# Kernel optimization log

Measured on AMD Instinct MI355X. Metric: run time of the kernel, lower is better.

Reference implementation:

```python
import jax, jax.numpy as jnp
import numpy as np

DIM = 128
HEADS = 4
K = 7          # neighborhood kernel size
MLP_RATIO = 4
EPS = 1e-5


def setup_inputs() -> dict:
    key = jax.random.key(0)
    ks = jax.random.split(key, 8)
    B, H, W, C = 4, 64, 64, DIM
    hid = C * MLP_RATIO
    s = lambda k, shape: jax.random.normal(k, shape, jnp.float32) * 0.02
    return {
        "x": jax.random.normal(ks[0], (B, H, W, C), jnp.float32),
        "ln1_g": jnp.ones((C,), jnp.float32),
        "ln1_b": jnp.zeros((C,), jnp.float32),
        "qkv_w": s(ks[1], (C, 3 * C)),
        "qkv_b": jnp.zeros((3 * C,), jnp.float32),
        "rpb": s(ks[2], (HEADS, 2 * K - 1, 2 * K - 1)),
        "proj_w": s(ks[3], (C, C)),
        "proj_b": jnp.zeros((C,), jnp.float32),
        "ln2_g": jnp.ones((C,), jnp.float32),
        "ln2_b": jnp.zeros((C,), jnp.float32),
        "fc1_w": s(ks[4], (C, hid)),
        "fc1_b": jnp.zeros((hid,), jnp.float32),
        "fc2_w": s(ks[5], (hid, C)),
        "fc2_b": jnp.zeros((C,), jnp.float32),
    }


def _ln(x, g, b):
    m = jnp.mean(x, axis=-1, keepdims=True)
    v = jnp.mean(jnp.square(x - m), axis=-1, keepdims=True)
    return (x - m) * jax.lax.rsqrt(v + EPS) * g + b


def _neigh_idx(L, k):
    # NATTEN border-clamped neighborhood: start = clamp(i - k//2, 0, L-k)
    i = jnp.arange(L)
    start = jnp.clip(i - k // 2, 0, L - k)
    idx = start[:, None] + jnp.arange(k)[None, :]        # [L, k] key positions
    rel = idx - i[:, None] + (k - 1)                     # [L, k] rpb indices in [0, 2k-2]
    return idx, rel


def _neighborhood_attention(x, qkv_w, qkv_b, rpb, proj_w, proj_b):
    B, H, W, C = x.shape
    nh, hd = HEADS, C // HEADS
    scale = hd ** -0.5
    qkv = (x @ qkv_w + qkv_b).reshape(B, H, W, 3, nh, hd)
    qkv = qkv.transpose(3, 0, 4, 1, 2, 5)                # [3, B, nh, H, W, hd]
    q, k_, v = qkv[0] * scale, qkv[1], qkv[2]
    ih, rh = _neigh_idx(H, K)
    iw, rw = _neigh_idx(W, K)
    # gather 7x7 neighborhoods: [B, nh, H, K, W, K, hd]
    kg = k_[:, :, ih][:, :, :, :, iw]
    vg = v[:, :, ih][:, :, :, :, iw]
    attn = jnp.einsum('bnywc,bnykxjc->bnyxkj', q, kg)    # [B, nh, H, W, K, K]
    bias = rpb[:, rh][:, :, :, rw]                       # [nh, H, K, W, K]
    attn = attn + bias.transpose(0, 1, 3, 2, 4)[None]
    a = jax.nn.softmax(attn.reshape(B, nh, H, W, K * K), axis=-1)
    a = a.reshape(B, nh, H, W, K, K)
    out = jnp.einsum('bnyxkj,bnykxjc->bnyxc', a, vg)     # [B, nh, H, W, hd]
    out = out.transpose(0, 2, 3, 1, 4).reshape(B, H, W, C)
    return out @ proj_w + proj_b


def reference(x, ln1_g, ln1_b, qkv_w, qkv_b, rpb, proj_w, proj_b,
              ln2_g, ln2_b, fc1_w, fc1_b, fc2_w, fc2_b):
    h = x + _neighborhood_attention(_ln(x, ln1_g, ln1_b), qkv_w, qkv_b, rpb, proj_w, proj_b)
    y = _ln(h, ln2_g, ln2_b)
    y = jax.nn.gelu(y @ fc1_w + fc1_b, approximate=False) @ fc2_w + fc2_b
    return h + y
```

## Files before the change

### kernel.cpp

```cpp
#include <hip/hip_runtime.h>
#include <math.h>

#define TOKS 16384
#define CDIM 128
#define NH 4
#define HD 32
#define HID 512
#define QSCALE 0.17677669529663687f
#define LEPS 1e-5f

typedef const float* fp;
typedef const unsigned short* bfp16;
typedef __attribute__((ext_vector_type(8))) short bf16x8;
typedef __attribute__((ext_vector_type(4))) float f32x4;

__device__ inline unsigned int bfp2(float a, float b) {
    unsigned int ua = __float_as_uint(a); ua = (ua + 0x7FFFu + ((ua >> 16) & 1u)) >> 16;
    unsigned int ub = __float_as_uint(b); ub = (ub + 0x7FFFu + ((ub >> 16) & 1u)) >> 16;
    return ua | (ub << 16);
}
__device__ inline unsigned short bf1(float a) {
    unsigned int u = __float_as_uint(a);
    return (unsigned short)((u + 0x7FFFu + ((u >> 16) & 1u)) >> 16);
}
__device__ inline float lo16(unsigned int u) { return __uint_as_float(u << 16); }
__device__ inline float hi16(unsigned int u) { return __uint_as_float(u & 0xFFFF0000u); }

__global__ __launch_bounds__(256) void prep(fp qw, fp pw, fp f1w, fp f2w,
                                            unsigned short* __restrict__ wt) {
    int e = blockIdx.x * 256 + threadIdx.x;
    float v;
    if (e < 49152)       { int n = e >> 7,  k = e & 127;          v = qw[(size_t)k * 384 + n]; }
    else if (e < 65536)  { int i = e - 49152;  int n = i >> 7, k = i & 127; v = pw[(size_t)k * 128 + n]; }
    else if (e < 131072) { int i = e - 65536;  int n = i >> 7, k = i & 127; v = f1w[(size_t)k * 512 + n]; }
    else                 { int i = e - 131072; int n = i >> 9, k = i & 511; v = f2w[(size_t)k * 128 + n]; }
    wt[e] = bf1(v);
}

__global__ __launch_bounds__(256) void k1_mfma(fp x, fp g1, fp b1, bfp16 wt0, fp wb,
                                               float* __restrict__ qb,
                                               unsigned short* __restrict__ kvb) {
    __shared__ unsigned int lds[12288];
    const int m0 = blockIdx.x * 128;
    const int nb = blockIdx.y * 64;
    const int tid = threadIdx.x;
#pragma unroll
    for (int i = 0; i < 8; i++) {
        int slot = tid + i * 256;
        int m = slot >> 4, c16 = slot & 15;
        const float4 v0 = *(const float4*)(x + (size_t)(m0 + m) * CDIM + c16 * 8);
        const float4 v1 = *(const float4*)(x + (size_t)(m0 + m) * CDIM + c16 * 8 + 4);
        float s = v0.x + v0.y + v0.z + v0.w + v1.x + v1.y + v1.z + v1.w;
        float q = v0.x * v0.x + v0.y * v0.y + v0.z * v0.z + v0.w * v0.w
                + v1.x * v1.x + v1.y * v1.y + v1.z * v1.z + v1.w * v1.w;
#pragma unroll
        for (int mm = 8; mm >= 1; mm >>= 1) { s += __shfl_xor(s, mm); q += __shfl_xor(q, mm); }
        float mu = s * (1.f / 128.f);
        float rs = rsqrtf(q * (1.f / 128.f) - mu * mu + LEPS);
        const float4 ga = *(const float4*)(g1 + c16 * 8);
        const float4 gb = *(const float4*)(g1 + c16 * 8 + 4);
        const float4 ba = *(const float4*)(b1 + c16 * 8);
        const float4 bb = *(const float4*)(b1 + c16 * 8 + 4);
        uint4 o;
        o.x = bfp2((v0.x - mu) * rs * ga.x + ba.x, (v0.y - mu) * rs * ga.y + ba.y);
        o.y = bfp2((v0.z - mu) * rs * ga.z + ba.z, (v0.w - mu) * rs * ga.w + ba.w);
        o.z = bfp2((v1.x - mu) * rs * gb.x + bb.x, (v1.y - mu) * rs * gb.y + bb.y);
        o.w = bfp2((v1.z - mu) * rs * gb.z + bb.z, (v1.w - mu) * rs * gb.w + bb.w);
        *(uint4*)&lds[m * 64 + ((c16 ^ (m & 15)) << 2)] = o;
    }
#pragma unroll
    for (int i = 0; i < 4; i++) {
        int slot = tid + i * 256;
        int n = slot >> 4, c16 = slot & 15;
        const uint4 v4 = *(const uint4*)(wt0 + (size_t)(nb + n) * 128 + c16 * 8);
        *(uint4*)&lds[8192 + n * 64 + (c16 ^ (n & 15)) * 4] = v4;
    }
    __syncthreads();

    const int lane = tid & 63, wid = tid >> 6, quad = lane >> 4, l16 = lane & 15;
    f32x4 acc[2][4];
#pragma unroll
    for (int mt = 0; mt < 2; mt++)
#pragma unroll
        for (int nt = 0; nt < 4; nt++) acc[mt][nt] = (f32x4){0.f, 0.f, 0.f, 0.f};
#pragma unroll
    for (int kk = 0; kk < 4; kk++) {
        int c = kk * 4 + quad;
        bf16x8 a0 = *(bf16x8*)&lds[(wid * 32 + l16) * 64 + (c ^ l16) * 4];
        bf16x8 a1 = *(bf16x8*)&lds[(wid * 32 + 16 + l16) * 64 + (c ^ l16) * 4];
#pragma unroll
        for (int nt = 0; nt < 4; nt++) {
            bf16x8 bf = *(bf16x8*)&lds[8192 + (nt * 16 + l16) * 64 + (c ^ l16) * 4];
            acc[0][nt] = __builtin_amdgcn_mfma_f32_16x16x32_bf16(a0, bf, acc[0][nt], 0, 0, 0);
            acc[1][nt] = __builtin_amdgcn_mfma_f32_16x16x32_bf16(a1, bf, acc[1][nt], 0, 0, 0);
        }
    }
#pragma unroll
    for (int nt = 0; nt < 4; nt++) {
        int col = nb + nt * 16 + l16;
        float bias = wb[col];
#pragma unroll
        for (int mt = 0; mt < 2; mt++)
#pragma unroll
            for (int r = 0; r < 4; r++) {
                int row = m0 + wid * 32 + mt * 16 + quad * 4 + r;
                float vres = acc[mt][nt][r] + bias;
                if (col < 128)
                    qb[(size_t)row * 128 + col] = vres * QSCALE;
                else if (col < 256)
                    kvb[(size_t)row * 256 + (col - 128)] = bf1(vres);
                else
                    kvb[(size_t)row * 256 + 128 + (col - 256)] = bf1(vres);
            }
    }
}

__global__ __launch_bounds__(512) void k2_attn(const float* __restrict__ qb,
                                               const unsigned short* __restrict__ kvb,
                                               fp rpb, unsigned short* __restrict__ attnb) {
    __shared__ unsigned int lds[25088];
    const int tile = blockIdx.x;
    const int bb = tile >> 6;
    const int ty0 = ((tile >> 3) & 7) << 3;
    const int tx0 = (tile & 7) << 3;
    const int ry0 = min(max(ty0 - 3, 0), 50);
    const int rx0 = min(max(tx0 - 3, 0), 50);
    const int tid = threadIdx.x;

#pragma unroll
    for (int it = 0; it < 13; it++) {
        int slot = it * 512 + tid;
        if (slot < 6272) {
            int r = slot >> 5, c = slot & 31;
            int i = r / 14, j = r - i * 14;
            const uint4 v = *(const uint4*)(kvb + (size_t)((bb << 12) + (ry0 + i) * 64 + rx0 + j) * 256 + c * 8);
            *(uint4*)&lds[r * 128 + ((c ^ (r & 7)) << 2)] = v;
        }
    }

    const int dh = tid & 1;
    const int head = (tid >> 1) & 3;
    const int t = tid >> 3;
    const int tx = t & 7, ty = t >> 3;
    const int y = ty0 + ty, x = tx0 + tx;
    const int token = (bb << 12) + y * 64 + x;
    const int sy = min(max(y - 3, 0), 57);
    const int sx = min(max(x - 3, 0), 57);
    const int ib = sy - ry0, jb = sx - rx0;
    const float* rp = rpb + head * 169 + (sy - y + 6) * 13 + (sx - x + 6);

    float q[16];
    {
        const float4* qp = (const float4*)(qb + (size_t)token * 128 + head * 32 + dh * 16);
        float4 a = qp[0], b = qp[1], c = qp[2], d = qp[3];
        q[0] = a.x; q[1] = a.y; q[2] = a.z; q[3] = a.w;
        q[4] = b.x; q[5] = b.y; q[6] = b.z; q[7] = b.w;
        q[8] = c.x; q[9] = c.y; q[10] = c.z; q[11] = c.w;
        q[12] = d.x; q[13] = d.y; q[14] = d.z; q[15] = d.w;
    }
    __syncthreads();

    const int cb = (head << 2) + (dh << 1);
    float m = -1e30f, l = 0.f;
    float o[16];
#pragma unroll
    for (int i2 = 0; i2 < 16; i2++) o[i2] = 0.f;

    for (int dy = 0; dy < 7; dy++) {
        float s[7];
#pragma unroll
        for (int dx = 0; dx < 7; dx++) {
            int r = (ib + dy) * 14 + jb + dx;
            int sw = r & 7;
            const uint4 k0 = *(const uint4*)&lds[r * 128 + ((cb ^ sw) << 2)];
            const uint4 k1 = *(const uint4*)&lds[r * 128 + (((cb + 1) ^ sw) << 2)];
            float ss = q[0] * lo16(k0.x) + q[1] * hi16(k0.x)
                     + q[2] * lo16(k0.y) + q[3] * hi16(k0.y)
                     + q[4] * lo16(k0.z) + q[5] * hi16(k0.z)
                     + q[6] * lo16(k0.w) + q[7] * hi16(k0.w)
                     + q[8] * lo16(k1.x) + q[9] * hi16(k1.x)
                     + q[10] * lo16(k1.y) + q[11] * hi16(k1.y)
                     + q[12] * lo16(k1.z) + q[13] * hi16(k1.z)
                     + q[14] * lo16(k1.w) + q[15] * hi16(k1.w);
            ss += __shfl_xor(ss, 1);
            s[dx] = ss + rp[dy * 13 + dx];
        }
        float rm = s[0];
#pragma unroll
        for (int dx = 1; dx < 7; dx++) rm = fmaxf(rm, s[dx]);
        float mn = fmaxf(m, rm);
        float cf = __expf(m - mn);
        l *= cf;
#pragma unroll
        for (int i2 = 0; i2 < 16; i2++) o[i2] *= cf;
#pragma unroll
        for (int dx = 0; dx < 7; dx++) {
            int r = (ib + dy) * 14 + jb + dx;
            int sw = r & 7;
            const uint4 v0 = *(const uint4*)&lds[r * 128 + (((cb + 16) ^ sw) << 2)];
            const uint4 v1 = *(const uint4*)&lds[r * 128 + (((cb + 17) ^ sw) << 2)];
            float p = __expf(s[dx] - mn);
            l += p;
            o[0] += p * lo16(v0.x); o[1] += p * hi16(v0.x);
            o[2] += p * lo16(v0.y); o[3] += p * hi16(v0.y);
            o[4] += p * lo16(v0.z); o[5] += p * hi16(v0.z);
            o[6] += p * lo16(v0.w); o[7] += p * hi16(v0.w);
            o[8] += p * lo16(v1.x); o[9] += p * hi16(v1.x);
            o[10] += p * lo16(v1.y); o[11] += p * hi16(v1.y);
            o[12] += p * lo16(v1.z); o[13] += p * hi16(v1.z);
            o[14] += p * lo16(v1.w); o[15] += p * hi16(v1.w);
        }
        m = mn;
    }
    float inv = 1.f / l;
    unsigned short* op = attnb + (size_t)token * 128 + head * 32 + dh * 16;
    uint4 ov;
    ov.x = bfp2(o[0] * inv, o[1] * inv); ov.y = bfp2(o[2] * inv, o[3] * inv);
    ov.z = bfp2(o[4] * inv, o[5] * inv); ov.w = bfp2(o[6] * inv, o[7] * inv);
    *(uint4*)op = ov;
    ov.x = bfp2(o[8] * inv, o[9] * inv); ov.y = bfp2(o[10] * inv, o[11] * inv);
    ov.z = bfp2(o[12] * inv, o[13] * inv); ov.w = bfp2(o[14] * inv, o[15] * inv);
    *(uint4*)(op + 8) = ov;
}

__global__ __launch_bounds__(256) void k3_mfma(bfp16 attnb, fp x, bfp16 wt1, fp pb,
                                               fp g2, fp b2,
                                               float* __restrict__ h,
                                               unsigned short* __restrict__ hn) {
    __shared__ unsigned int lds[12288];
    const int m0 = blockIdx.x * 64;
    const int tid = threadIdx.x;
#pragma unroll
    for (int i = 0; i < 4; i++) {
        int slot = tid + i * 256;
        int m = slot >> 4, c16 = slot & 15;
        const uint4 v4 = *(const uint4*)(attnb + (size_t)(m0 + m) * CDIM + c16 * 8);
        *(uint4*)&lds[m * 64 + (c16 ^ (m & 15)) * 4] = v4;
    }
#pragma unroll
    for (int i = 0; i < 8; i++) {
        int slot = tid + i * 256;
        int n = slot >> 4, c16 = slot & 15;
        const uint4 v4 = *(const uint4*)(wt1 + (size_t)n * 128 + c16 * 8);
        *(uint4*)&lds[4096 + n * 64 + (c16 ^ (n & 15)) * 4] = v4;
    }
    __syncthreads();

    const int lane = tid & 63, wid = tid >> 6, quad = lane >> 4, l16 = lane & 15;
    const int mrow = wid * 16 + l16;
    f32x4 acc[8];
#pragma unroll
    for (int nt = 0; nt < 8; nt++) acc[nt] = (f32x4){0.f, 0.f, 0.f, 0.f};
#pragma unroll
    for (int kk = 0; kk < 4; kk++) {
        int c = kk * 4 + quad;
        bf16x8 a = *(bf16x8*)&lds[mrow * 64 + (c ^ l16) * 4];
#pragma unroll
        for (int nt = 0; nt < 8; nt++) {
            bf16x8 bf = *(bf16x8*)&lds[4096 + (nt * 16 + l16) * 64 + (c ^ l16) * 4];
            acc[nt] = __builtin_amdgcn_mfma_f32_16x16x32_bf16(a, bf, acc[nt], 0, 0, 0);
        }
    }
    float s[4] = {0.f, 0.f, 0.f, 0.f}, q[4] = {0.f, 0.f, 0.f, 0.f};
#pragma unroll
    for (int nt = 0; nt < 8; nt++) {
        int col = nt * 16 + l16;
        float bias = pb[col];
#pragma unroll
        for (int r = 0; r < 4; r++) {
            int row = m0 + wid * 16 + quad * 4 + r;
            float hv = x[(size_t)row * CDIM + col] + acc[nt][r] + bias;
            h[(size_t)row * CDIM + col] = hv;
            acc[nt][r] = hv;
            s[r] += hv; q[r] += hv * hv;
        }
    }
#pragma unroll
    for (int m = 1; m <= 8; m <<= 1) {
#pragma unroll
        for (int r = 0; r < 4; r++) {
            s[r] += __shfl_xor(s[r], m);
            q[r] += __shfl_xor(q[r], m);
        }
    }
    float mu[4], rs[4];
#pragma unroll
    for (int r = 0; r < 4; r++) {
        mu[r] = s[r] * (1.f / 128.f);
        rs[r] = rsqrtf(q[r] * (1.f / 128.f) - mu[r] * mu[r] + LEPS);
    }
#pragma unroll
    for (int nt = 0; nt < 8; nt++) {
        int col = nt * 16 + l16;
        float gg = g2[col], bb = b2[col];
#pragma unroll
        for (int r = 0; r < 4; r++) {
            int row = m0 + wid * 16 + quad * 4 + r;
            hn[(size_t)row * CDIM + col] = bf1((acc[nt][r] - mu[r]) * rs[r] * gg + bb);
        }
    }
}

__global__ __launch_bounds__(256) void kmlp3(bfp16 hn, bfp16 wt2, fp b1v, bfp16 wt3, fp b2v,
                                             fp h, float* __restrict__ out) {
    __shared__ unsigned int lds[10240];
    const int m0 = blockIdx.x * 32;
    const int tid = threadIdx.x;
#pragma unroll
    for (int i = 0; i < 2; i++) {
        int slot = tid + i * 256;
        int m = slot >> 4, c16 = slot & 15;
        const uint4 v4 = *(const uint4*)(hn + (size_t)(m0 + m) * CDIM + c16 * 8);
        *(uint4*)&lds[m * 64 + ((c16 ^ (m & 15)) << 2)] = v4;
    }
    __syncthreads();

    const int lane = tid & 63, wid = tid >> 6, quad = lane >> 4, l16 = lane & 15;

#pragma unroll
    for (int ht = 0; ht < 8; ht++) {
        const int hrow = wid * 128 + ht * 16 + l16;
        f32x4 acc0 = (f32x4){0.f, 0.f, 0.f, 0.f};
        f32x4 acc1 = (f32x4){0.f, 0.f, 0.f, 0.f};
#pragma unroll
        for (int kk = 0; kk < 4; kk++) {
            int c = kk * 4 + quad;
            bf16x8 wf = *(const bf16x8*)(wt2 + (size_t)hrow * 128 + kk * 32 + quad * 8);
            bf16x8 x0 = *(bf16x8*)&lds[l16 * 64 + ((c ^ l16) << 2)];
            bf16x8 x1 = *(bf16x8*)&lds[(16 + l16) * 64 + ((c ^ l16) << 2)];
            acc0 = __builtin_amdgcn_mfma_f32_16x16x32_bf16(wf, x0, acc0, 0, 0, 0);
            acc1 = __builtin_amdgcn_mfma_f32_16x16x32_bf16(wf, x1, acc1, 0, 0, 0);
        }
        const int hidb = wid * 128 + ht * 16 + quad * 4;
        const float4 bb = *(const float4*)(b1v + hidb);
        const int c16y = hidb >> 3;
        const int woff = (quad & 1) << 1;
#pragma unroll
        for (int t = 0; t < 2; t++) {
            f32x4 a = t ? acc1 : acc0;
            int row = t * 16 + l16;
            float z0 = a[0] + bb.x, z1 = a[1] + bb.y, z2 = a[2] + bb.z, z3 = a[3] + bb.w;
            float g0 = 0.5f * z0 * (1.f + erff(z0 * 0.70710678118654752f));
            float g1 = 0.5f * z1 * (1.f + erff(z1 * 0.70710678118654752f));
            float g2 = 0.5f * z2 * (1.f + erff(z2 * 0.70710678118654752f));
            float g3 = 0.5f * z3 * (1.f + erff(z3 * 0.70710678118654752f));
            uint2 val; val.x = bfp2(g0, g1); val.y = bfp2(g2, g3);
            *(uint2*)&lds[2048 + row * 256 + ((c16y ^ (row & 15)) << 2) + woff] = val;
        }
    }
    __syncthreads();

    f32x4 acc2[2][2];
#pragma unroll
    for (int mt = 0; mt < 2; mt++)
#pragma unroll
        for (int nt = 0; nt < 2; nt++) acc2[mt][nt] = (f32x4){0.f, 0.f, 0.f, 0.f};
#pragma unroll
    for (int kc = 0; kc < 16; kc++) {
        int c = kc * 4 + quad;
        bf16x8 a0 = *(bf16x8*)&lds[2048 + l16 * 256 + ((c ^ l16) << 2)];
        bf16x8 a1 = *(bf16x8*)&lds[2048 + (16 + l16) * 256 + ((c ^ l16) << 2)];
#pragma unroll
        for (int nt = 0; nt < 2; nt++) {
            int crow = wid * 32 + nt * 16 + l16;
            bf16x8 bf = *(const bf16x8*)(wt3 + (size_t)crow * 512 + kc * 32 + quad * 8);
            acc2[0][nt] = __builtin_amdgcn_mfma_f32_16x16x32_bf16(a0, bf, acc2[0][nt], 0, 0, 0);
            acc2[1][nt] = __builtin_amdgcn_mfma_f32_16x16x32_bf16(a1, bf, acc2[1][nt], 0, 0, 0);
        }
    }
#pragma unroll
    for (int nt = 0; nt < 2; nt++) {
        int col = wid * 32 + nt * 16 + l16;
        float bias = b2v[col];
#pragma unroll
        for (int mt = 0; mt < 2; mt++)
#pragma unroll
            for (int r = 0; r < 4; r++) {
                int row = m0 + mt * 16 + quad * 4 + r;
                out[(size_t)row * CDIM + col] = h[(size_t)row * CDIM + col] + acc2[mt][nt][r] + bias;
            }
    }
}

extern "C" void kernel_launch(void* const* d_in, const int* in_sizes, int n_in,
                              void* d_out, int out_size, void* d_ws, size_t ws_size,
                              hipStream_t stream) {
    fp x      = (fp)d_in[0];
    fp ln1_g  = (fp)d_in[1];
    fp ln1_b  = (fp)d_in[2];
    fp qkv_w  = (fp)d_in[3];
    fp qkv_b  = (fp)d_in[4];
    fp rpb    = (fp)d_in[5];
    fp proj_w = (fp)d_in[6];
    fp proj_b = (fp)d_in[7];
    fp ln2_g  = (fp)d_in[8];
    fp ln2_b  = (fp)d_in[9];
    fp fc1_w  = (fp)d_in[10];
    fp fc1_b  = (fp)d_in[11];
    fp fc2_w  = (fp)d_in[12];
    fp fc2_b  = (fp)d_in[13];
    float* out = (float*)d_out;

    float* ws = (float*)d_ws;
    float* h  = ws;
    unsigned short* xn = (unsigned short*)(h + (size_t)TOKS * CDIM);
    unsigned short* hn = xn + (size_t)TOKS * CDIM;
    float* qb = (float*)(hn + (size_t)TOKS * CDIM);
    unsigned short* kvb   = (unsigned short*)(qb + (size_t)TOKS * CDIM);
    unsigned short* attnb = kvb + (size_t)TOKS * 256;
    unsigned short* wt    = attnb + (size_t)TOKS * CDIM;

    unsigned short* wt0 = wt;
    unsigned short* wt1 = wt + 49152;
    unsigned short* wt2 = wt + 65536;
    unsigned short* wt3 = wt + 131072;

    prep<<<768, 256, 0, stream>>>(qkv_w, proj_w, fc1_w, fc2_w, wt);
    k1_mfma<<<dim3(TOKS / 128, 6), 256, 0, stream>>>(x, ln1_g, ln1_b, wt0, qkv_b, qb, kvb);
    k2_attn<<<TOKS / 64, 512, 0, stream>>>(qb, kvb, rpb, attnb);
    k3_mfma<<<TOKS / 64, 256, 0, stream>>>(attnb, x, wt1, proj_b, ln2_g, ln2_b, h, hn);
    kmlp3<<<TOKS / 32, 256, 0, stream>>>(hn, wt2, fc1_b, wt3, fc2_b, h, out);
}
```

Measured before the change: 143.9 us.

## Fuse output projection, residual and LayerNorm2 into the neighborhood attention kernel

The attention kernel now stages its per-tile 64x128 bf16 output in LDS together with the projection weights, which are prefetched into registers at kernel start. Half the threads then run the MFMA projection, add the residual, compute LayerNorm2 and write h and hn directly. This drops the separate k3 launch and the global round trip of the attention output. In exchange it adds register pressure in the attention kernel, and the epilogue runs on only 256 of 512 threads, which may reduce occupancy or overlap.

```diff
diff --git a/kernel.cpp b/kernel.cpp
--- a/kernel.cpp
+++ b/kernel.cpp
@@ -117,7 +117,10 @@
 
 __global__ __launch_bounds__(512) void k2_attn(const float* __restrict__ qb,
                                                const unsigned short* __restrict__ kvb,
-                                               fp rpb, unsigned short* __restrict__ attnb) {
+                                               fp rpb, fp x, bfp16 wt1, fp pb,
+                                               fp g2, fp b2,
+                                               float* __restrict__ h,
+                                               unsigned short* __restrict__ hn) {
     __shared__ unsigned int lds[25088];
     const int tile = blockIdx.x;
     const int bb = tile >> 6;
@@ -126,6 +129,12 @@
     const int ry0 = min(max(ty0 - 3, 0), 50);
     const int rx0 = min(max(tx0 - 3, 0), 50);
     const int tid = threadIdx.x;
+    const int base = (bb << 12) + ty0 * 64 + tx0;
+
+    uint4 wreg[4];
+#pragma unroll
+    for (int i = 0; i < 4; i++)
+        wreg[i] = *(const uint4*)(wt1 + (size_t)(tid + i * 512) * 8);
 
 #pragma unroll
     for (int it = 0; it < 13; it++) {
@@ -142,12 +151,12 @@
     const int head = (tid >> 1) & 3;
     const int t = tid >> 3;
     const int tx = t & 7, ty = t >> 3;
-    const int y = ty0 + ty, x = tx0 + tx;
-    const int token = (bb << 12) + y * 64 + x;
+    const int y = ty0 + ty, xx2 = tx0 + tx;
+    const int token = (bb << 12) + y * 64 + xx2;
     const int sy = min(max(y - 3, 0), 57);
-    const int sx = min(max(x - 3, 0), 57);
+    const int sx = min(max(xx2 - 3, 0), 57);
     const int ib = sy - ry0, jb = sx - rx0;
-    const float* rp = rpb + head * 169 + (sy - y + 6) * 13 + (sx - x + 6);
+    const float* rp = rpb + head * 169 + (sy - y + 6) * 13 + (sx - xx2 + 6);
 
     float q[16];
     {
@@ -213,90 +222,79 @@
         m = mn;
     }
     float inv = 1.f / l;
-    unsigned short* op = attnb + (size_t)token * 128 + head * 32 + dh * 16;
-    uint4 ov;
-    ov.x = bfp2(o[0] * inv, o[1] * inv); ov.y = bfp2(o[2] * inv, o[3] * inv);
-    ov.z = bfp2(o[4] * inv, o[5] * inv); ov.w = bfp2(o[6] * inv, o[7] * inv);
-    *(uint4*)op = ov;
-    ov.x = bfp2(o[8] * inv, o[9] * inv); ov.y = bfp2(o[10] * inv, o[11] * inv);
-    ov.z = bfp2(o[12] * inv, o[13] * inv); ov.w = bfp2(o[14] * inv, o[15] * inv);
-    *(uint4*)(op + 8) = ov;
-}
-
-__global__ __launch_bounds__(256) void k3_mfma(bfp16 attnb, fp x, bfp16 wt1, fp pb,
-                                               fp g2, fp b2,
-                                               float* __restrict__ h,
-                                               unsigned short* __restrict__ hn) {
-    __shared__ unsigned int lds[12288];
-    const int m0 = blockIdx.x * 64;
-    const int tid = threadIdx.x;
+    uint4 ov0, ov1;
+    ov0.x = bfp2(o[0] * inv, o[1] * inv);  ov0.y = bfp2(o[2] * inv, o[3] * inv);
+    ov0.z = bfp2(o[4] * inv, o[5] * inv);  ov0.w = bfp2(o[6] * inv, o[7] * inv);
+    ov1.x = bfp2(o[8] * inv, o[9] * inv);  ov1.y = bfp2(o[10] * inv, o[11] * inv);
+    ov1.z = bfp2(o[12] * inv, o[13] * inv); ov1.w = bfp2(o[14] * inv, o[15] * inv);
+
+    __syncthreads();
+    *(uint4*)&lds[t * 64 + ((cb ^ (t & 15)) << 2)] = ov0;
+    *(uint4*)&lds[t * 64 + (((cb + 1) ^ (t & 15)) << 2)] = ov1;
 #pragma unroll
     for (int i = 0; i < 4; i++) {
-        int slot = tid + i * 256;
-        int m = slot >> 4, c16 = slot & 15;
-        const uint4 v4 = *(const uint4*)(attnb + (size_t)(m0 + m) * CDIM + c16 * 8);
-        *(uint4*)&lds[m * 64 + (c16 ^ (m & 15)) * 4] = v4;
-    }
-#pragma unroll
-    for (int i = 0; i < 8; i++) {
-        int slot = tid + i * 256;
+        int slot = tid + i * 512;
         int n = slot >> 4, c16 = slot & 15;
-        const uint4 v4 = *(const uint4*)(wt1 + (size_t)n * 128 + c16 * 8);
-        *(uint4*)&lds[4096 + n * 64 + (c16 ^ (n & 15)) * 4] = v4;
-    }
-    __syncthreads();
-
-    const int lane = tid & 63, wid = tid >> 6, quad = lane >> 4, l16 = lane & 15;
-    const int mrow = wid * 16 + l16;
-    f32x4 acc[8];
-#pragma unroll
-    for (int nt = 0; nt < 8; nt++) acc[nt] = (f32x4){0.f, 0.f, 0.f, 0.f};
-#pragma unroll
-    for (int kk = 0; kk < 4; kk++) {
-        int c = kk * 4 + quad;
-        bf16x8 a = *(bf16x8*)&lds[mrow * 64 + (c ^ l16) * 4];
+        *(uint4*)&lds[4096 + n * 64 + ((c16 ^ (n & 15)) << 2)] = wreg[i];
+    }
+    __syncthreads();
+
+    if (tid < 256) {
+        const int lane2 = tid & 63, wid2 = tid >> 6, quad2 = lane2 >> 4, l162 = lane2 & 15;
+        const int mrow = wid2 * 16 + l162;
+        f32x4 acc[8];
+#pragma unroll
+        for (int nt = 0; nt < 8; nt++) acc[nt] = (f32x4){0.f, 0.f, 0.f, 0.f};
+#pragma unroll
+        for (int kk = 0; kk < 4; kk++) {
+            int c = kk * 4 + quad2;
+            bf16x8 a = *(bf16x8*)&lds[mrow * 64 + ((c ^ l162) << 2)];
+#pragma unroll
+            for (int nt = 0; nt < 8; nt++) {
+                bf16x8 bf = *(bf16x8*)&lds[4096 + (nt * 16 + l162) * 64 + ((c ^ l162) << 2)];
+                acc[nt] = __builtin_amdgcn_mfma_f32_16x16x32_bf16(a, bf, acc[nt], 0, 0, 0);
+            }
+        }
+        float s2[4] = {0.f, 0.f, 0.f, 0.f}, q2[4] = {0.f, 0.f, 0.f, 0.f};
+        int grow[4];
+#pragma unroll
+        for (int r = 0; r < 4; r++) {
+            int lt = wid2 * 16 + quad2 * 4 + r;
+            grow[r] = base + ((lt >> 3) << 6) + (lt & 7);
+        }
 #pragma unroll
         for (int nt = 0; nt < 8; nt++) {
-            bf16x8 bf = *(bf16x8*)&lds[4096 + (nt * 16 + l16) * 64 + (c ^ l16) * 4];
-            acc[nt] = __builtin_amdgcn_mfma_f32_16x16x32_bf16(a, bf, acc[nt], 0, 0, 0);
-        }
-    }
-    float s[4] = {0.f, 0.f, 0.f, 0.f}, q[4] = {0.f, 0.f, 0.f, 0.f};
-#pragma unroll
-    for (int nt = 0; nt < 8; nt++) {
-        int col = nt * 16 + l16;
-        float bias = pb[col];
+            int col = nt * 16 + l162;
+            float bias = pb[col];
+#pragma unroll
+            for (int r = 0; r < 4; r++) {
+                float hv = x[(size_t)grow[r] * CDIM + col] + acc[nt][r] + bias;
+                h[(size_t)grow[r] * CDIM + col] = hv;
+                acc[nt][r] = hv;
+                s2[r] += hv; q2[r] += hv * hv;
+            }
+        }
+#pragma unroll
+        for (int mm = 1; mm <= 8; mm <<= 1) {
+#pragma unroll
+            for (int r = 0; r < 4; r++) {
+                s2[r] += __shfl_xor(s2[r], mm);
+                q2[r] += __shfl_xor(q2[r], mm);
+            }
+        }
+        float mu[4], rs[4];
 #pragma unroll
         for (int r = 0; r < 4; r++) {
-            int row = m0 + wid * 16 + quad * 4 + r;
-            float hv = x[(size_t)row * CDIM + col] + acc[nt][r] + bias;
-            h[(size_t)row * CDIM + col] = hv;
-            acc[nt][r] = hv;
-            s[r] += hv; q[r] += hv * hv;
-        }
-    }
-#pragma unroll
-    for (int m = 1; m <= 8; m <<= 1) {
-#pragma unroll
-        for (int r = 0; r < 4; r++) {
-            s[r] += __shfl_xor(s[r], m);
-            q[r] += __shfl_xor(q[r], m);
-        }
-    }
-    float mu[4], rs[4];
-#pragma unroll
-    for (int r = 0; r < 4; r++) {
-        mu[r] = s[r] * (1.f / 128.f);
-        rs[r] = rsqrtf(q[r] * (1.f / 128.f) - mu[r] * mu[r] + LEPS);
-    }
-#pragma unroll
-    for (int nt = 0; nt < 8; nt++) {
-        int col = nt * 16 + l16;
-        float gg = g2[col], bb = b2[col];
-#pragma unroll
-        for (int r = 0; r < 4; r++) {
-            int row = m0 + wid * 16 + quad * 4 + r;
-            hn[(size_t)row * CDIM + col] = bf1((acc[nt][r] - mu[r]) * rs[r] * gg + bb);
+            mu[r] = s2[r] * (1.f / 128.f);
+            rs[r] = rsqrtf(q2[r] * (1.f / 128.f) - mu[r] * mu[r] + LEPS);
+        }
+#pragma unroll
+        for (int nt = 0; nt < 8; nt++) {
+            int col = nt * 16 + l162;
+            float gg = g2[col], bbv = b2[col];
+#pragma unroll
+            for (int r = 0; r < 4; r++)
+                hn[(size_t)grow[r] * CDIM + col] = bf1((acc[nt][r] - mu[r]) * rs[r] * gg + bbv);
         }
     }
 }
@@ -417,7 +415,6 @@
 
     prep<<<768, 256, 0, stream>>>(qkv_w, proj_w, fc1_w, fc2_w, wt);
     k1_mfma<<<dim3(TOKS / 128, 6), 256, 0, stream>>>(x, ln1_g, ln1_b, wt0, qkv_b, qb, kvb);
-    k2_attn<<<TOKS / 64, 512, 0, stream>>>(qb, kvb, rpb, attnb);
-    k3_mfma<<<TOKS / 64, 256, 0, stream>>>(attnb, x, wt1, proj_b, ln2_g, ln2_b, h, hn);
+    k2_attn<<<TOKS / 64, 512, 0, stream>>>(qb, kvb, rpb, x, wt1, proj_b, ln2_g, ln2_b, h, hn);
     kmlp3<<<TOKS / 32, 256, 0, stream>>>(hn, wt2, fc1_b, wt3, fc2_b, h, out);
 }
```

Result: slower. 164.1 us (+14.0%).

## Split neighborhood attention blocks per head with smaller LDS tiles

Applied to the files above, without the earlier changes.

The attention kernel now launches one block per (tile, head) pair instead of one block covering all four heads. Each block stages only that head's K/V slice (8 KB per row tile instead of 32 KB) into shared memory and uses 256 threads, with each head-dim quarter handled by one thread and a two-step shuffle reduction. This aims to raise occupancy and block count (smaller LDS, fewer registers) at the cost of an extra shuffle and more, smaller global loads of the halo region.

```diff
diff --git a/kernel.cpp b/kernel.cpp
--- a/kernel.cpp
+++ b/kernel.cpp
@@ -115,11 +115,13 @@
     }
 }
 
-__global__ __launch_bounds__(512) void k2_attn(const float* __restrict__ qb,
+__global__ __launch_bounds__(256) void k2_attn(const float* __restrict__ qb,
                                                const unsigned short* __restrict__ kvb,
                                                fp rpb, unsigned short* __restrict__ attnb) {
-    __shared__ unsigned int lds[25088];
-    const int tile = blockIdx.x;
+    __shared__ unsigned int lds[6272];
+    const int blk = blockIdx.x;
+    const int head = blk & 3;
+    const int tile = blk >> 2;
     const int bb = tile >> 6;
     const int ty0 = ((tile >> 3) & 7) << 3;
     const int tx0 = (tile & 7) << 3;
@@ -128,19 +130,20 @@
     const int tid = threadIdx.x;
 
 #pragma unroll
-    for (int it = 0; it < 13; it++) {
-        int slot = it * 512 + tid;
-        if (slot < 6272) {
-            int r = slot >> 5, c = slot & 31;
+    for (int it = 0; it < 7; it++) {
+        int slot = it * 256 + tid;
+        if (slot < 1568) {
+            int r = slot >> 3, c = slot & 7;
             int i = r / 14, j = r - i * 14;
-            const uint4 v = *(const uint4*)(kvb + (size_t)((bb << 12) + (ry0 + i) * 64 + rx0 + j) * 256 + c * 8);
-            *(uint4*)&lds[r * 128 + ((c ^ (r & 7)) << 2)] = v;
-        }
-    }
-
-    const int dh = tid & 1;
-    const int head = (tid >> 1) & 3;
-    const int t = tid >> 3;
+            size_t tok = (size_t)((bb << 12) + (ry0 + i) * 64 + rx0 + j);
+            int off = (c < 4) ? (head * 32 + c * 8) : (128 + head * 32 + (c - 4) * 8);
+            const uint4 v = *(const uint4*)(kvb + tok * 256 + off);
+            *(uint4*)&lds[r * 32 + ((c ^ (r & 7)) << 2)] = v;
+        }
+    }
+
+    const int dh = tid & 3;
+    const int t = tid >> 2;
     const int tx = t & 7, ty = t >> 3;
     const int y = ty0 + ty, x = tx0 + tx;
     const int token = (bb << 12) + y * 64 + x;
@@ -149,40 +152,32 @@
     const int ib = sy - ry0, jb = sx - rx0;
     const float* rp = rpb + head * 169 + (sy - y + 6) * 13 + (sx - x + 6);
 
-    float q[16];
+    float q[8];
     {
-        const float4* qp = (const float4*)(qb + (size_t)token * 128 + head * 32 + dh * 16);
-        float4 a = qp[0], b = qp[1], c = qp[2], d = qp[3];
-        q[0] = a.x; q[1] = a.y; q[2] = a.z; q[3] = a.w;
-        q[4] = b.x; q[5] = b.y; q[6] = b.z; q[7] = b.w;
-        q[8] = c.x; q[9] = c.y; q[10] = c.z; q[11] = c.w;
-        q[12] = d.x; q[13] = d.y; q[14] = d.z; q[15] = d.w;
+        const float4* qp = (const float4*)(qb + (size_t)token * 128 + head * 32 + dh * 8);
+        float4 q0 = qp[0], q1 = qp[1];
+        q[0] = q0.x; q[1] = q0.y; q[2] = q0.z; q[3] = q0.w;
+        q[4] = q1.x; q[5] = q1.y; q[6] = q1.z; q[7] = q1.w;
     }
     __syncthreads();
 
-    const int cb = (head << 2) + (dh << 1);
     float m = -1e30f, l = 0.f;
-    float o[16];
-#pragma unroll
-    for (int i2 = 0; i2 < 16; i2++) o[i2] = 0.f;
+    float o[8];
+#pragma unroll
+    for (int i2 = 0; i2 < 8; i2++) o[i2] = 0.f;
 
     for (int dy = 0; dy < 7; dy++) {
         float s[7];
 #pragma unroll
         for (int dx = 0; dx < 7; dx++) {
             int r = (ib + dy) * 14 + jb + dx;
-            int sw = r & 7;
-            const uint4 k0 = *(const uint4*)&lds[r * 128 + ((cb ^ sw) << 2)];
-            const uint4 k1 = *(const uint4*)&lds[r * 128 + (((cb + 1) ^ sw) << 2)];
-            float ss = q[0] * lo16(k0.x) + q[1] * hi16(k0.x)
-                     + q[2] * lo16(k0.y) + q[3] * hi16(k0.y)
-                     + q[4] * lo16(k0.z) + q[5] * hi16(k0.z)
-                     + q[6] * lo16(k0.w) + q[7] * hi16(k0.w)
-                     + q[8] * lo16(k1.x) + q[9] * hi16(k1.x)
-                     + q[10] * lo16(k1.y) + q[11] * hi16(k1.y)
-                     + q[12] * lo16(k1.z) + q[13] * hi16(k1.z)
-                     + q[14] * lo16(k1.w) + q[15] * hi16(k1.w);
+            const uint4 kk = *(const uint4*)&lds[r * 32 + ((dh ^ (r & 7)) << 2)];
+            float ss = q[0] * lo16(kk.x) + q[1] * hi16(kk.x)
+                     + q[2] * lo16(kk.y) + q[3] * hi16(kk.y)
+                     + q[4] * lo16(kk.z) + q[5] * hi16(kk.z)
+                     + q[6] * lo16(kk.w) + q[7] * hi16(kk.w);
             ss += __shfl_xor(ss, 1);
+            ss += __shfl_xor(ss, 2);
             s[dx] = ss + rp[dy * 13 + dx];
         }
         float rm = s[0];
@@ -192,35 +187,25 @@
         float cf = __expf(m - mn);
         l *= cf;
 #pragma unroll
-        for (int i2 = 0; i2 < 16; i2++) o[i2] *= cf;
+        for (int i2 = 0; i2 < 8; i2++) o[i2] *= cf;
 #pragma unroll
         for (int dx = 0; dx < 7; dx++) {
             int r = (ib + dy) * 14 + jb + dx;
-            int sw = r & 7;
-            const uint4 v0 = *(const uint4*)&lds[r * 128 + (((cb + 16) ^ sw) << 2)];
-            const uint4 v1 = *(const uint4*)&lds[r * 128 + (((cb + 17) ^ sw) << 2)];
+            const uint4 vv = *(const uint4*)&lds[r * 32 + (((4 + dh) ^ (r & 7)) << 2)];
             float p = __expf(s[dx] - mn);
             l += p;
-            o[0] += p * lo16(v0.x); o[1] += p * hi16(v0.x);
-            o[2] += p * lo16(v0.y); o[3] += p * hi16(v0.y);
-            o[4] += p * lo16(v0.z); o[5] += p * hi16(v0.z);
-            o[6] += p * lo16(v0.w); o[7] += p * hi16(v0.w);
-            o[8] += p * lo16(v1.x); o[9] += p * hi16(v1.x);
-            o[10] += p * lo16(v1.y); o[11] += p * hi16(v1.y);
-            o[12] += p * lo16(v1.z); o[13] += p * hi16(v1.z);
-            o[14] += p * lo16(v1.w); o[15] += p * hi16(v1.w);
+            o[0] += p * lo16(vv.x); o[1] += p * hi16(vv.x);
+            o[2] += p * lo16(vv.y); o[3] += p * hi16(vv.y);
+            o[4] += p * lo16(vv.z); o[5] += p * hi16(vv.z);
+            o[6] += p * lo16(vv.w); o[7] += p * hi16(vv.w);
         }
         m = mn;
     }
     float inv = 1.f / l;
-    unsigned short* op = attnb + (size_t)token * 128 + head * 32 + dh * 16;
     uint4 ov;
     ov.x = bfp2(o[0] * inv, o[1] * inv); ov.y = bfp2(o[2] * inv, o[3] * inv);
     ov.z = bfp2(o[4] * inv, o[5] * inv); ov.w = bfp2(o[6] * inv, o[7] * inv);
-    *(uint4*)op = ov;
-    ov.x = bfp2(o[8] * inv, o[9] * inv); ov.y = bfp2(o[10] * inv, o[11] * inv);
-    ov.z = bfp2(o[12] * inv, o[13] * inv); ov.w = bfp2(o[14] * inv, o[15] * inv);
-    *(uint4*)(op + 8) = ov;
+    *(uint4*)(attnb + (size_t)token * 128 + head * 32 + dh * 8) = ov;
 }
 
 __global__ __launch_bounds__(256) void k3_mfma(bfp16 attnb, fp x, bfp16 wt1, fp pb,
@@ -417,7 +402,7 @@
 
     prep<<<768, 256, 0, stream>>>(qkv_w, proj_w, fc1_w, fc2_w, wt);
     k1_mfma<<<dim3(TOKS / 128, 6), 256, 0, stream>>>(x, ln1_g, ln1_b, wt0, qkv_b, qb, kvb);
-    k2_attn<<<TOKS / 64, 512, 0, stream>>>(qb, kvb, rpb, attnb);
+    k2_attn<<<TOKS / 64 * NH, 256, 0, stream>>>(qb, kvb, rpb, attnb);
     k3_mfma<<<TOKS / 64, 256, 0, stream>>>(attnb, x, wt1, proj_b, ln2_g, ln2_b, h, hn);
     kmlp3<<<TOKS / 32, 256, 0, stream>>>(hn, wt2, fc1_b, wt3, fc2_b, h, out);
 }
```

Measured after the change: 147.4 us. 2.5% more time.

## Fuse projection+LN2 kernel with MLP kernel, keeping residual and normed tile in LDS

Applied to the files above, without the earlier changes.

Merges the attention output projection, residual add and LayerNorm2 into the MLP kernel, so each 32-token block computes h and its normalized bf16 copy in shared memory rather than writing them to global memory and reading them back. LN row statistics are now split across two waves per row half and combined through LDS. This removes one kernel launch and the global round trip for h (fp32) and hn (bf16). In exchange, proj weights are read straight from global memory instead of being staged in LDS, and the larger LDS footprint may reduce occupancy.

```diff
diff --git a/kernel.cpp b/kernel.cpp
--- a/kernel.cpp
+++ b/kernel.cpp
@@ -223,99 +223,93 @@
     *(uint4*)(op + 8) = ov;
 }
 
-__global__ __launch_bounds__(256) void k3_mfma(bfp16 attnb, fp x, bfp16 wt1, fp pb,
-                                               fp g2, fp b2,
-                                               float* __restrict__ h,
-                                               unsigned short* __restrict__ hn) {
-    __shared__ unsigned int lds[12288];
-    const int m0 = blockIdx.x * 64;
+__global__ __launch_bounds__(256) void kpm(bfp16 attnb, fp x, bfp16 wt1, fp pb,
+                                           fp g2, fp b2, bfp16 wt2, fp b1v,
+                                           bfp16 wt3, fp b2v, float* __restrict__ out) {
+    __shared__ unsigned int lds[16384];
+    float* ldsf = (float*)lds;
+    unsigned short* ldsu = (unsigned short*)lds;
+    const int m0 = blockIdx.x * 32;
     const int tid = threadIdx.x;
-#pragma unroll
-    for (int i = 0; i < 4; i++) {
+    const int lane = tid & 63, wid = tid >> 6, quad = lane >> 4, l16 = lane & 15;
+
+#pragma unroll
+    for (int i = 0; i < 2; i++) {
         int slot = tid + i * 256;
         int m = slot >> 4, c16 = slot & 15;
         const uint4 v4 = *(const uint4*)(attnb + (size_t)(m0 + m) * CDIM + c16 * 8);
-        *(uint4*)&lds[m * 64 + (c16 ^ (m & 15)) * 4] = v4;
-    }
-#pragma unroll
-    for (int i = 0; i < 8; i++) {
-        int slot = tid + i * 256;
-        int n = slot >> 4, c16 = slot & 15;
-        const uint4 v4 = *(const uint4*)(wt1 + (size_t)n * 128 + c16 * 8);
-        *(uint4*)&lds[4096 + n * 64 + (c16 ^ (n & 15)) * 4] = v4;
-    }
-    __syncthreads();
-
-    const int lane = tid & 63, wid = tid >> 6, quad = lane >> 4, l16 = lane & 15;
-    const int mrow = wid * 16 + l16;
-    f32x4 acc[8];
-#pragma unroll
-    for (int nt = 0; nt < 8; nt++) acc[nt] = (f32x4){0.f, 0.f, 0.f, 0.f};
+        *(uint4*)&lds[m * 64 + ((c16 ^ (m & 15)) << 2)] = v4;
+    }
+    __syncthreads();
+
+    const int mt = wid & 1, nhf = wid >> 1;
+    f32x4 pacc[4];
+#pragma unroll
+    for (int nt = 0; nt < 4; nt++) pacc[nt] = (f32x4){0.f, 0.f, 0.f, 0.f};
 #pragma unroll
     for (int kk = 0; kk < 4; kk++) {
         int c = kk * 4 + quad;
-        bf16x8 a = *(bf16x8*)&lds[mrow * 64 + (c ^ l16) * 4];
-#pragma unroll
-        for (int nt = 0; nt < 8; nt++) {
-            bf16x8 bf = *(bf16x8*)&lds[4096 + (nt * 16 + l16) * 64 + (c ^ l16) * 4];
-            acc[nt] = __builtin_amdgcn_mfma_f32_16x16x32_bf16(a, bf, acc[nt], 0, 0, 0);
-        }
-    }
-    float s[4] = {0.f, 0.f, 0.f, 0.f}, q[4] = {0.f, 0.f, 0.f, 0.f};
-#pragma unroll
-    for (int nt = 0; nt < 8; nt++) {
-        int col = nt * 16 + l16;
+        bf16x8 a = *(bf16x8*)&lds[(mt * 16 + l16) * 64 + ((c ^ l16) << 2)];
+#pragma unroll
+        for (int nt = 0; nt < 4; nt++) {
+            int crow = nhf * 64 + nt * 16 + l16;
+            bf16x8 bf = *(const bf16x8*)(wt1 + (size_t)crow * 128 + kk * 32 + quad * 8);
+            pacc[nt] = __builtin_amdgcn_mfma_f32_16x16x32_bf16(a, bf, pacc[nt], 0, 0, 0);
+        }
+    }
+    float sr[4] = {0.f, 0.f, 0.f, 0.f}, qr[4] = {0.f, 0.f, 0.f, 0.f};
+#pragma unroll
+    for (int nt = 0; nt < 4; nt++) {
+        int col = nhf * 64 + nt * 16 + l16;
         float bias = pb[col];
 #pragma unroll
         for (int r = 0; r < 4; r++) {
-            int row = m0 + wid * 16 + quad * 4 + r;
-            float hv = x[(size_t)row * CDIM + col] + acc[nt][r] + bias;
-            h[(size_t)row * CDIM + col] = hv;
-            acc[nt][r] = hv;
-            s[r] += hv; q[r] += hv * hv;
-        }
-    }
-#pragma unroll
-    for (int m = 1; m <= 8; m <<= 1) {
+            int lrow = mt * 16 + quad * 4 + r;
+            float hv = x[(size_t)(m0 + lrow) * CDIM + col] + pacc[nt][r] + bias;
+            ldsf[4096 + lrow * 128 + col] = hv;
+            pacc[nt][r] = hv;
+            sr[r] += hv; qr[r] += hv * hv;
+        }
+    }
+#pragma unroll
+    for (int mm = 1; mm <= 8; mm <<= 1) {
 #pragma unroll
         for (int r = 0; r < 4; r++) {
-            s[r] += __shfl_xor(s[r], m);
-            q[r] += __shfl_xor(q[r], m);
-        }
-    }
+            sr[r] += __shfl_xor(sr[r], mm);
+            qr[r] += __shfl_xor(qr[r], mm);
+        }
+    }
+    __syncthreads();
+    if (l16 == 0) {
+#pragma unroll
+        for (int r = 0; r < 4; r++) {
+            ldsf[wid * 32 + (quad * 4 + r) * 2]     = sr[r];
+            ldsf[wid * 32 + (quad * 4 + r) * 2 + 1] = qr[r];
+        }
+    }
+    __syncthreads();
     float mu[4], rs[4];
 #pragma unroll
     for (int r = 0; r < 4; r++) {
-        mu[r] = s[r] * (1.f / 128.f);
-        rs[r] = rsqrtf(q[r] * (1.f / 128.f) - mu[r] * mu[r] + LEPS);
-    }
-#pragma unroll
-    for (int nt = 0; nt < 8; nt++) {
-        int col = nt * 16 + l16;
-        float gg = g2[col], bb = b2[col];
+        int po = (wid ^ 2) * 32 + (quad * 4 + r) * 2;
+        float st = sr[r] + ldsf[po];
+        float qt = qr[r] + ldsf[po + 1];
+        mu[r] = st * (1.f / 128.f);
+        rs[r] = rsqrtf(qt * (1.f / 128.f) - mu[r] * mu[r] + LEPS);
+    }
+#pragma unroll
+    for (int nt = 0; nt < 4; nt++) {
+        int col = nhf * 64 + nt * 16 + l16;
+        float gg = g2[col], bbv = b2[col];
+        int c16h = col >> 3, cw = col & 7;
 #pragma unroll
         for (int r = 0; r < 4; r++) {
-            int row = m0 + wid * 16 + quad * 4 + r;
-            hn[(size_t)row * CDIM + col] = bf1((acc[nt][r] - mu[r]) * rs[r] * gg + bb);
-        }
-    }
-}
-
-__global__ __launch_bounds__(256) void kmlp3(bfp16 hn, bfp16 wt2, fp b1v, bfp16 wt3, fp b2v,
-                                             fp h, float* __restrict__ out) {
-    __shared__ unsigned int lds[10240];
-    const int m0 = blockIdx.x * 32;
-    const int tid = threadIdx.x;
-#pragma unroll
-    for (int i = 0; i < 2; i++) {
-        int slot = tid + i * 256;
-        int m = slot >> 4, c16 = slot & 15;
-        const uint4 v4 = *(const uint4*)(hn + (size_t)(m0 + m) * CDIM + c16 * 8);
-        *(uint4*)&lds[m * 64 + ((c16 ^ (m & 15)) << 2)] = v4;
-    }
-    __syncthreads();
-
-    const int lane = tid & 63, wid = tid >> 6, quad = lane >> 4, l16 = lane & 15;
+            int lrow = mt * 16 + quad * 4 + r;
+            ldsu[4096 + lrow * 128 + ((c16h ^ (lrow & 15)) << 3) + cw] =
+                bf1((pacc[nt][r] - mu[r]) * rs[r] * gg + bbv);
+        }
+    }
+    __syncthreads();
 
 #pragma unroll
     for (int ht = 0; ht < 8; ht++) {
@@ -326,8 +320,8 @@
         for (int kk = 0; kk < 4; kk++) {
             int c = kk * 4 + quad;
             bf16x8 wf = *(const bf16x8*)(wt2 + (size_t)hrow * 128 + kk * 32 + quad * 8);
-            bf16x8 x0 = *(bf16x8*)&lds[l16 * 64 + ((c ^ l16) << 2)];
-            bf16x8 x1 = *(bf16x8*)&lds[(16 + l16) * 64 + ((c ^ l16) << 2)];
+            bf16x8 x0 = *(bf16x8*)&lds[2048 + l16 * 64 + ((c ^ l16) << 2)];
+            bf16x8 x1 = *(bf16x8*)&lds[2048 + (16 + l16) * 64 + ((c ^ l16) << 2)];
             acc0 = __builtin_amdgcn_mfma_f32_16x16x32_bf16(wf, x0, acc0, 0, 0, 0);
             acc1 = __builtin_amdgcn_mfma_f32_16x16x32_bf16(wf, x1, acc1, 0, 0, 0);
         }
@@ -342,24 +336,24 @@
             float z0 = a[0] + bb.x, z1 = a[1] + bb.y, z2 = a[2] + bb.z, z3 = a[3] + bb.w;
             float g0 = 0.5f * z0 * (1.f + erff(z0 * 0.70710678118654752f));
             float g1 = 0.5f * z1 * (1.f + erff(z1 * 0.70710678118654752f));
-            float g2 = 0.5f * z2 * (1.f + erff(z2 * 0.70710678118654752f));
+            float g2v = 0.5f * z2 * (1.f + erff(z2 * 0.70710678118654752f));
             float g3 = 0.5f * z3 * (1.f + erff(z3 * 0.70710678118654752f));
-            uint2 val; val.x = bfp2(g0, g1); val.y = bfp2(g2, g3);
-            *(uint2*)&lds[2048 + row * 256 + ((c16y ^ (row & 15)) << 2) + woff] = val;
+            uint2 val; val.x = bfp2(g0, g1); val.y = bfp2(g2v, g3);
+            *(uint2*)&lds[8192 + row * 256 + ((c16y ^ (row & 15)) << 2) + woff] = val;
         }
     }
     __syncthreads();
 
     f32x4 acc2[2][2];
 #pragma unroll
-    for (int mt = 0; mt < 2; mt++)
-#pragma unroll
-        for (int nt = 0; nt < 2; nt++) acc2[mt][nt] = (f32x4){0.f, 0.f, 0.f, 0.f};
+    for (int mt2 = 0; mt2 < 2; mt2++)
+#pragma unroll
+        for (int nt = 0; nt < 2; nt++) acc2[mt2][nt] = (f32x4){0.f, 0.f, 0.f, 0.f};
 #pragma unroll
     for (int kc = 0; kc < 16; kc++) {
         int c = kc * 4 + quad;
-        bf16x8 a0 = *(bf16x8*)&lds[2048 + l16 * 256 + ((c ^ l16) << 2)];
-        bf16x8 a1 = *(bf16x8*)&lds[2048 + (16 + l16) * 256 + ((c ^ l16) << 2)];
+        bf16x8 a0 = *(bf16x8*)&lds[8192 + l16 * 256 + ((c ^ l16) << 2)];
+        bf16x8 a1 = *(bf16x8*)&lds[8192 + (16 + l16) * 256 + ((c ^ l16) << 2)];
 #pragma unroll
         for (int nt = 0; nt < 2; nt++) {
             int crow = wid * 32 + nt * 16 + l16;
@@ -373,11 +367,12 @@
         int col = wid * 32 + nt * 16 + l16;
         float bias = b2v[col];
 #pragma unroll
-        for (int mt = 0; mt < 2; mt++)
+        for (int mt2 = 0; mt2 < 2; mt2++)
 #pragma unroll
             for (int r = 0; r < 4; r++) {
-                int row = m0 + mt * 16 + quad * 4 + r;
-                out[(size_t)row * CDIM + col] = h[(size_t)row * CDIM + col] + acc2[mt][nt][r] + bias;
+                int lrow = mt2 * 16 + quad * 4 + r;
+                out[(size_t)(m0 + lrow) * CDIM + col] =
+                    ldsf[4096 + lrow * 128 + col] + acc2[mt2][nt][r] + bias;
             }
     }
 }
@@ -418,6 +413,6 @@
     prep<<<768, 256, 0, stream>>>(qkv_w, proj_w, fc1_w, fc2_w, wt);
     k1_mfma<<<dim3(TOKS / 128, 6), 256, 0, stream>>>(x, ln1_g, ln1_b, wt0, qkv_b, qb, kvb);
     k2_attn<<<TOKS / 64, 512, 0, stream>>>(qb, kvb, rpb, attnb);
-    k3_mfma<<<TOKS / 64, 256, 0, stream>>>(attnb, x, wt1, proj_b, ln2_g, ln2_b, h, hn);
-    kmlp3<<<TOKS / 32, 256, 0, stream>>>(hn, wt2, fc1_b, wt3, fc2_b, h, out);
-}
+    kpm<<<TOKS / 32, 256, 0, stream>>>(attnb, x, wt1, proj_b, ln2_g, ln2_b,
+                                       wt2, fc1_b, wt3, fc2_b, out);
+}
```

Measured after the change: 140.2 us. 2.6% less time.
